# Kernel tuning notes

Measured on AMD Instinct MI355X. Metric: run time of the kernel, lower is better.

Reference implementation:

```python
import jax, jax.numpy as jnp
import numpy as np

N_ROUTINGS = 3


def squash(v, axis=-1):
    sn = jnp.sum(jnp.square(v), axis=axis, keepdims=True)
    return (jnp.sqrt(sn) / (1.0 + sn)) * v


def setup_inputs() -> dict:
    key = jax.random.key(0)
    k1, k2 = jax.random.split(key)
    B, R, C, n_in, d_in = 16, 14, 14, 64, 16
    n_caps, caps_dim = 10, 16
    inputs = jax.random.normal(k1, (B, R, C, n_in, d_in), dtype=jnp.float32)
    W = jax.random.normal(k2, (n_caps, n_in, d_in, caps_dim), dtype=jnp.float32) * 0.1
    return {"inputs": inputs, "W": W}


def reference(inputs, W):
    # inputs: [B,R,C,i,e], W: [n,i,e,o] -> res (u_hat): [B,R,C,n,i,o]
    res = jnp.einsum('brcie,nieo->brcnio', inputs, W)
    n_in = inputs.shape[3]
    # softmax of zeros over last axis -> uniform 1/n_in
    b = jnp.full(res.shape[:-1], 1.0 / n_in, dtype=res.dtype)  # [B,R,C,n,i]
    for _ in range(N_ROUTINGS - 1):
        v = squash(jnp.sum(b[..., None] * res, axis=-2))  # [B,R,C,n,o]
        b = b + jnp.sum(res * v[..., None, :], axis=-1)   # agreement
    out = squash(jnp.sum(b[..., None] * res, axis=-2))
    return out  # [B,R,C,n_caps,caps_dim]
```

## Files before the change

### kernel.cpp

```cpp
#include <hip/hip_runtime.h>
#include <hip/hip_bf16.h>

typedef __attribute__((ext_vector_type(4))) float f32x4;
typedef __attribute__((ext_vector_type(8))) short s16x8;

#define GLOBAL_AS __attribute__((address_space(1)))
#define LDS_AS    __attribute__((address_space(3)))

#define QPB 8


template<int CTRL>
__device__ __forceinline__ float dpp_add(float x) {
    int v = __builtin_amdgcn_update_dpp(0, __float_as_int(x), CTRL, 0xF, 0xF, true);
    return x + __int_as_float(v);
}

__device__ __forceinline__ void stage_inp(const float* gq, char* ldst, int tid) {
#pragma unroll
    for (int k = 0; k < 4; ++k) {
        int d  = k * 256 + tid;
        int p  = d >> 8;
        int cd = d & 255;
        int c  = cd ^ ((cd >> 3) & 7);
        __builtin_amdgcn_global_load_lds(
            (const GLOBAL_AS unsigned int*)(gq + (p * 256 + c) * 4),
            (LDS_AS unsigned int*)(ldst + d * 16), 16, 0, 0);
    }
}

__global__ __launch_bounds__(256, 4) void caps_kernel(
    const float* __restrict__ inp,
    const float* __restrict__ W,
    float* __restrict__ out)
{
    const int tid = threadIdx.x;
    const int w   = tid >> 6;
    const int l   = tid & 63;
    const int n   = blockIdx.x / 98;
    const int qg  = blockIdx.x % 98;
    const int q0  = qg * QPB;

    extern __shared__ __align__(16) char smem[];
    float* inp0  = (float*)smem;
    float* inp1  = (float*)(smem + 16384);
    char*  res_s = smem + 32768;
    float* Wq    = inp0;

    const int i4 = l >> 2;
    const int oq = l & 3;
    const int i_ = w * 16 + i4;

    stage_inp(inp + (size_t)q0 * 4096, (char*)inp1, tid);

    const float* Wn = W + (size_t)n * 16384;
    f32x4 w_regs[16];
    for (int k = 0; k < 4; ++k) {
#pragma unroll
        for (int k2 = 0; k2 < 4; ++k2) {
            int d  = k2 * 256 + tid;
            int ir = d >> 6;
            int cd = d & 63;
            int c  = cd ^ (ir & 7);
            __builtin_amdgcn_global_load_lds(
                (const GLOBAL_AS unsigned int*)(Wn + (k * 1024 + ir * 64 + c) * 4),
                (LDS_AS unsigned int*)((char*)Wq + d * 16), 16, 0, 0);
        }
        __syncthreads();
        if (w == k) {
#pragma unroll
            for (int e = 0; e < 16; ++e)
                w_regs[e] = *(const f32x4*)(Wq + i4 * 256 + (((e * 4 + oq) ^ (i4 & 7)) << 2));
        }
        __syncthreads();
    }

    const int col = l & 15;
    const int kg  = l >> 4;

    s16x8 ones;
#pragma unroll
    for (int j = 0; j < 8; ++j) ones[j] = (short)0x3F80;

#pragma unroll 2
    for (int t = 0; t < QPB; ++t) {
        const int q = q0 + t;
        const float* buf = (t & 1) ? inp0 : inp1;
        if (t + 1 < QPB)
            stage_inp(inp + (size_t)(q + 1) * 4096,
                      (t & 1) ? (char*)inp1 : (char*)inp0, tid);

#pragma unroll
        for (int p = 0; p < 4; ++p) {
            f32x4 a[4];
#pragma unroll
            for (int eq = 0; eq < 4; ++eq) {
                int c = i_ * 4 + eq;
                a[eq] = *(const f32x4*)(buf + p * 1024 + ((c ^ ((i_ >> 1) & 7)) << 2));
            }
            f32x4 acc = (f32x4)0.0f;
#pragma unroll
            for (int e = 0; e < 16; ++e)
                acc += a[e >> 2][e & 3] * w_regs[e];
#pragma unroll
            for (int d = 0; d < 4; ++d) {
                int o = oq * 4 + d;
                __hip_bfloat16 b = __float2bfloat16(acc[d]);
                int byte = p * 2048 + o * 128 + (((i_ >> 3) ^ (o & 7)) << 4) + (i_ & 7) * 2;
                *(unsigned short*)(res_s + byte) = *(unsigned short*)&b;
            }
        }

        asm volatile("s_waitcnt lgkmcnt(0)" ::: "memory");
        __builtin_amdgcn_s_barrier();
        asm volatile("" ::: "memory");
        __builtin_amdgcn_sched_barrier(0);

        s16x8 fr0 = *(const s16x8*)(res_s + w * 2048 + col * 128 + (((kg + 0) ^ (col & 7)) << 4));
        s16x8 fr1 = *(const s16x8*)(res_s + w * 2048 + col * 128 + (((kg + 4) ^ (col & 7)) << 4));

        f32x4 G  = (f32x4)0.0f;
        f32x4 C2 = (f32x4)0.0f;
        G  = __builtin_amdgcn_mfma_f32_16x16x32_bf16(fr0, fr0, G, 0, 0, 0);
        G  = __builtin_amdgcn_mfma_f32_16x16x32_bf16(fr1, fr1, G, 0, 0, 0);
        C2 = __builtin_amdgcn_mfma_f32_16x16x32_bf16(ones, fr0, C2, 0, 0, 0);
        C2 = __builtin_amdgcn_mfma_f32_16x16x32_bf16(ones, fr1, C2, 0, 0, 0);

        float s = C2[0] * (1.0f / 64.0f);

#pragma unroll
        for (int it = 0; it < 2; ++it) {
            float sn = s * s;
            sn = dpp_add<0xB1>(sn);
            sn = dpp_add<0x4E>(sn);
            sn = dpp_add<0x124>(sn);
            sn = dpp_add<0x128>(sn);
            float scale = sqrtf(sn) / (1.0f + sn);
            float v = scale * s;
            float v0 = __shfl(v, kg * 4 + 0);
            float v1 = __shfl(v, kg * 4 + 1);
            float v2 = __shfl(v, kg * 4 + 2);
            float v3 = __shfl(v, kg * 4 + 3);
            float acc2 = G[0] * v0 + G[1] * v1 + G[2] * v2 + G[3] * v3;
            acc2 += __shfl_xor(acc2, 16);
            acc2 += __shfl_xor(acc2, 32);
            s += acc2;
        }

        float sn = s * s;
        sn = dpp_add<0xB1>(sn);
        sn = dpp_add<0x4E>(sn);
        sn = dpp_add<0x124>(sn);
        sn = dpp_add<0x128>(sn);
        float scale = sqrtf(sn) / (1.0f + sn);
        float v = scale * s;

        asm volatile("s_waitcnt vmcnt(0)" ::: "memory");
        __builtin_amdgcn_s_barrier();
        asm volatile("" ::: "memory");
        __builtin_amdgcn_sched_barrier(0);

        if (l < 16)
            out[((size_t)(q * 4 + w) * 10 + n) * 16 + col] = v;
    }
}

extern "C" void kernel_launch(void* const* d_in, const int* in_sizes, int n_in,
                              void* d_out, int out_size, void* d_ws, size_t ws_size,
                              hipStream_t stream) {
    const float* inp = (const float*)d_in[0];
    const float* W   = (const float*)d_in[1];
    float* out = (float*)d_out;

    dim3 grid(980), block(256);
    hipLaunchKernelGGL(caps_kernel, grid, block, 40960, stream, inp, W, out);
}
```

Measured before the change: 34.28 us.

## Load inputs directly to registers and use DPP lane rotation instead of LDS staging

Replaces the LDS double-buffered input staging with coalesced direct global loads into registers, prefetched one position ahead. Each lane now holds only its own four input values and takes the other e-values from neighbouring lanes through DPP rotations, with W registers pre-rotated to match. The result buffer is double-buffered, which removes the trailing barrier per iteration. LDS use drops to 32KB, while launch bounds fall to 3 waves per EU to allow more registers for the prefetch, which may reduce occupancy.

```diff
diff --git a/kernel.cpp b/kernel.cpp
--- a/kernel.cpp
+++ b/kernel.cpp
@@ -6,7 +6,6 @@
 
 #define GLOBAL_AS __attribute__((address_space(1)))
 #define LDS_AS    __attribute__((address_space(3)))
-
 #define QPB 8
 
 
@@ -15,21 +14,12 @@
     int v = __builtin_amdgcn_update_dpp(0, __float_as_int(x), CTRL, 0xF, 0xF, true);
     return x + __int_as_float(v);
 }
-
-__device__ __forceinline__ void stage_inp(const float* gq, char* ldst, int tid) {
-#pragma unroll
-    for (int k = 0; k < 4; ++k) {
-        int d  = k * 256 + tid;
-        int p  = d >> 8;
-        int cd = d & 255;
-        int c  = cd ^ ((cd >> 3) & 7);
-        __builtin_amdgcn_global_load_lds(
-            (const GLOBAL_AS unsigned int*)(gq + (p * 256 + c) * 4),
-            (LDS_AS unsigned int*)(ldst + d * 16), 16, 0, 0);
-    }
+template<int CTRL>
+__device__ __forceinline__ float dpp_movf(float x) {
+    return __int_as_float(__builtin_amdgcn_update_dpp(0, __float_as_int(x), CTRL, 0xF, 0xF, true));
 }
 
-__global__ __launch_bounds__(256, 4) void caps_kernel(
+__global__ __launch_bounds__(256, 3) void caps_kernel(
     const float* __restrict__ inp,
     const float* __restrict__ W,
     float* __restrict__ out)
@@ -42,19 +32,22 @@
     const int q0  = qg * QPB;
 
     extern __shared__ __align__(16) char smem[];
-    float* inp0  = (float*)smem;
-    float* inp1  = (float*)(smem + 16384);
-    char*  res_s = smem + 32768;
-    float* Wq    = inp0;
+    char*  res_s = smem;
+    float* W_s   = (float*)(smem + 16384);
 
     const int i4 = l >> 2;
     const int oq = l & 3;
     const int i_ = w * 16 + i4;
+    const int col = l & 15;
+    const int kg  = l >> 4;
 
-    stage_inp(inp + (size_t)q0 * 4096, (char*)inp1, tid);
+    f32x4 raw[4], rawn[4];
+#pragma unroll
+    for (int p = 0; p < 4; ++p)
+        raw[p] = *(const f32x4*)(inp + (size_t)q0 * 4096 + p * 1024 + w * 256 + l * 4);
 
     const float* Wn = W + (size_t)n * 16384;
-    f32x4 w_regs[16];
+    f32x4 wrot[16];
     for (int k = 0; k < 4; ++k) {
 #pragma unroll
         for (int k2 = 0; k2 < 4; ++k2) {
@@ -64,19 +57,23 @@
             int c  = cd ^ (ir & 7);
             __builtin_amdgcn_global_load_lds(
                 (const GLOBAL_AS unsigned int*)(Wn + (k * 1024 + ir * 64 + c) * 4),
-                (LDS_AS unsigned int*)((char*)Wq + d * 16), 16, 0, 0);
+                (LDS_AS unsigned int*)((char*)W_s + d * 16), 16, 0, 0);
         }
         __syncthreads();
         if (w == k) {
 #pragma unroll
-            for (int e = 0; e < 16; ++e)
-                w_regs[e] = *(const f32x4*)(Wq + i4 * 256 + (((e * 4 + oq) ^ (i4 & 7)) << 2));
+            for (int r = 0; r < 4; ++r) {
+                int c = (oq + r) & 3;
+#pragma unroll
+                for (int kk = 0; kk < 4; ++kk) {
+                    int e = c * 4 + kk;
+                    wrot[r * 4 + kk] =
+                        *(const f32x4*)(W_s + i4 * 256 + (((e * 4 + oq) ^ (i4 & 7)) << 2));
+                }
+            }
         }
         __syncthreads();
     }
-
-    const int col = l & 15;
-    const int kg  = l >> 4;
 
     s16x8 ones;
 #pragma unroll
@@ -85,29 +82,42 @@
 #pragma unroll 2
     for (int t = 0; t < QPB; ++t) {
         const int q = q0 + t;
-        const float* buf = (t & 1) ? inp0 : inp1;
-        if (t + 1 < QPB)
-            stage_inp(inp + (size_t)(q + 1) * 4096,
-                      (t & 1) ? (char*)inp1 : (char*)inp0, tid);
+        char* rbuf = res_s + (t & 1) * 8192;
+
+        if (t + 1 < QPB) {
+#pragma unroll
+            for (int p = 0; p < 4; ++p)
+                rawn[p] = *(const f32x4*)(inp + (size_t)(q + 1) * 4096 + p * 1024 + w * 256 + l * 4);
+        }
 
 #pragma unroll
         for (int p = 0; p < 4; ++p) {
-            f32x4 a[4];
-#pragma unroll
-            for (int eq = 0; eq < 4; ++eq) {
-                int c = i_ * 4 + eq;
-                a[eq] = *(const f32x4*)(buf + p * 1024 + ((c ^ ((i_ >> 1) & 7)) << 2));
-            }
+            f32x4 a = raw[p];
             f32x4 acc = (f32x4)0.0f;
 #pragma unroll
-            for (int e = 0; e < 16; ++e)
-                acc += a[e >> 2][e & 3] * w_regs[e];
+            for (int kk = 0; kk < 4; ++kk) acc += a[kk] * wrot[kk];
+            f32x4 b1;
 #pragma unroll
-            for (int d = 0; d < 4; ++d) {
-                int o = oq * 4 + d;
-                __hip_bfloat16 b = __float2bfloat16(acc[d]);
+            for (int kk = 0; kk < 4; ++kk) b1[kk] = dpp_movf<0x39>(a[kk]);
+#pragma unroll
+            for (int kk = 0; kk < 4; ++kk) acc += b1[kk] * wrot[4 + kk];
+            f32x4 b2;
+#pragma unroll
+            for (int kk = 0; kk < 4; ++kk) b2[kk] = dpp_movf<0x4E>(a[kk]);
+#pragma unroll
+            for (int kk = 0; kk < 4; ++kk) acc += b2[kk] * wrot[8 + kk];
+            f32x4 b3;
+#pragma unroll
+            for (int kk = 0; kk < 4; ++kk) b3[kk] = dpp_movf<0x93>(a[kk]);
+#pragma unroll
+            for (int kk = 0; kk < 4; ++kk) acc += b3[kk] * wrot[12 + kk];
+
+#pragma unroll
+            for (int dd = 0; dd < 4; ++dd) {
+                int o = oq * 4 + dd;
+                __hip_bfloat16 bb = __float2bfloat16(acc[dd]);
                 int byte = p * 2048 + o * 128 + (((i_ >> 3) ^ (o & 7)) << 4) + (i_ & 7) * 2;
-                *(unsigned short*)(res_s + byte) = *(unsigned short*)&b;
+                *(unsigned short*)(rbuf + byte) = *(unsigned short*)&bb;
             }
         }
 
@@ -116,8 +126,8 @@
         asm volatile("" ::: "memory");
         __builtin_amdgcn_sched_barrier(0);
 
-        s16x8 fr0 = *(const s16x8*)(res_s + w * 2048 + col * 128 + (((kg + 0) ^ (col & 7)) << 4));
-        s16x8 fr1 = *(const s16x8*)(res_s + w * 2048 + col * 128 + (((kg + 4) ^ (col & 7)) << 4));
+        s16x8 fr0 = *(const s16x8*)(rbuf + w * 2048 + col * 128 + (((kg + 0) ^ (col & 7)) << 4));
+        s16x8 fr1 = *(const s16x8*)(rbuf + w * 2048 + col * 128 + (((kg + 4) ^ (col & 7)) << 4));
 
         f32x4 G  = (f32x4)0.0f;
         f32x4 C2 = (f32x4)0.0f;
@@ -141,10 +151,10 @@
             float v1 = __shfl(v, kg * 4 + 1);
             float v2 = __shfl(v, kg * 4 + 2);
             float v3 = __shfl(v, kg * 4 + 3);
-            float acc2 = G[0] * v0 + G[1] * v1 + G[2] * v2 + G[3] * v3;
-            acc2 += __shfl_xor(acc2, 16);
-            acc2 += __shfl_xor(acc2, 32);
-            s += acc2;
+            float acc = G[0] * v0 + G[1] * v1 + G[2] * v2 + G[3] * v3;
+            acc += __shfl_xor(acc, 16);
+            acc += __shfl_xor(acc, 32);
+            s += acc;
         }
 
         float sn = s * s;
@@ -155,13 +165,13 @@
         float scale = sqrtf(sn) / (1.0f + sn);
         float v = scale * s;
 
-        asm volatile("s_waitcnt vmcnt(0)" ::: "memory");
-        __builtin_amdgcn_s_barrier();
-        asm volatile("" ::: "memory");
-        __builtin_amdgcn_sched_barrier(0);
-
         if (l < 16)
             out[((size_t)(q * 4 + w) * 10 + n) * 16 + col] = v;
+
+        if (t + 1 < QPB) {
+#pragma unroll
+            for (int p = 0; p < 4; ++p) raw[p] = rawn[p];
+        }
     }
 }
 
@@ -173,5 +183,5 @@
     float* out = (float*)d_out;
 
     dim3 grid(980), block(256);
-    hipLaunchKernelGGL(caps_kernel, grid, block, 40960, stream, inp, W, out);
+    hipLaunchKernelGGL(caps_kernel, grid, block, 32768, stream, inp, W, out);
 }
```

Measured after the change: 36.39 us. +6.2%, slower.
